# Optimization experiments

Hardware: AMD Instinct MI355X
Metric: run time of the kernel (lower is better)

Reference implementation:

```python
import jax, jax.numpy as jnp
import numpy as np

B, N, K = 16, 2048, 20
EPS = 1e-5
SLOPE = 0.2  # LeakyReLU negative slope


def _lrelu(x):
    return jnp.where(x >= 0, x, SLOPE * x)


def _bn(x, g, b, axes):
    # BatchNorm in training mode (batch statistics), channel-last layout
    m = x.mean(axes, keepdims=True)
    v = x.var(axes, keepdims=True)
    return (x - m) * jax.lax.rsqrt(v + EPS) * g + b


def _graph_features(pts, k):
    # pts: [B, N, C] -> edge features [B, N, k, 2C] = concat(x_j - x_i, x_i)
    xx = jnp.sum(pts * pts, axis=-1)                       # [B, N]
    inner = jnp.einsum('bnc,bmc->bnm', pts, pts)           # [B, N, N]
    neg_d = 2.0 * inner - xx[:, :, None] - xx[:, None, :]  # -||x_i - x_j||^2
    _, idx = jax.lax.top_k(neg_d, k)                       # [B, N, k]
    xj = jax.vmap(lambda p, i: p[i])(pts, idx)             # [B, N, k, C]
    xi = pts[:, :, None, :]                                # [B, N, 1, C]
    return jnp.concatenate([xj - xi, jnp.broadcast_to(xi, xj.shape)], axis=-1)


def _forward(x, conv_w, conv_g, conv_b, w1, b1, g1, bt1, w2, b2, g2, bt2,
             w3, b3, g3, bt3, w4, b4, w5, b5):
    feat = _graph_features(x, K)                           # [B, N, K, 6]
    # 1x1 Conv2d (bias=False) + BN2d + LeakyReLU, then max over neighbors
    h = jnp.einsum('bnkc,oc->bnko', feat, conv_w)          # [B, N, K, 64]
    h = _lrelu(_bn(h, conv_g, conv_b, (0, 1, 2)))
    h = h.max(axis=2)                                      # [B, N, 64]
    # DBR blocks: Linear + BN1d + LeakyReLU over points
    h = _lrelu(_bn(h @ w1 + b1, g1, bt1, (0, 1)))          # [B, N, 64]
    h = _lrelu(_bn(h @ w2 + b2, g2, bt2, (0, 1)))          # [B, N, 128]
    h = _lrelu(_bn(h @ w3 + b3, g3, bt3, (0, 1)))          # [B, N, 128]
    h = h.max(axis=1)                                      # MaxChannel -> [B, 128]
    h = _lrelu(h @ w4 + b4)                                # DbR -> [B, 512]
    return h @ w5 + b5                                     # [B, 2*Z_DIM=256]


def setup_inputs() -> dict:
    key = jax.random.key(0)
    ks = jax.random.split(key, 8)
    rn = lambda k, s, sc: (jax.random.normal(k, s, jnp.float32) * sc)
    return {
        'x': jax.random.normal(ks[0], (B, N, 3), jnp.float32),
        'conv_w': rn(ks[1], (64, 6), 0.3),
        'conv_g': jnp.ones(64, jnp.float32), 'conv_b': jnp.zeros(64, jnp.float32),
        'w1': rn(ks[2], (64, 64), 0.1), 'b1': jnp.zeros(64, jnp.float32),
        'g1': jnp.ones(64, jnp.float32), 'bt1': jnp.zeros(64, jnp.float32),
        'w2': rn(ks[3], (64, 128), 0.1), 'b2': jnp.zeros(128, jnp.float32),
        'g2': jnp.ones(128, jnp.float32), 'bt2': jnp.zeros(128, jnp.float32),
        'w3': rn(ks[4], (128, 128), 0.1), 'b3': jnp.zeros(128, jnp.float32),
        'g3': jnp.ones(128, jnp.float32), 'bt3': jnp.zeros(128, jnp.float32),
        'w4': rn(ks[5], (128, 512), 0.05), 'b4': jnp.zeros(512, jnp.float32),
        'w5': rn(ks[6], (512, 256), 0.05), 'b5': jnp.zeros(256, jnp.float32),
    }


def reference(x, conv_w, conv_g, conv_b, w1, b1, g1, bt1, w2, b2, g2, bt2,
              w3, b3, g3, bt3, w4, b4, w5, b5):
    return _forward(x, conv_w, conv_g, conv_b, w1, b1, g1, bt1, w2, b2, g2, bt2,
                    w3, b3, g3, bt3, w4, b4, w5, b5)
```

## Files before the change

### kernel.cpp

```cpp
#include <hip/hip_runtime.h>
#include <math.h>

#define NB   16
#define NPTS 2048
#define KNBR 20
#define NROWS (NB*NPTS)
#define CONV_M ((double)(NB)*(double)(NPTS)*(double)(KNBR))
#define ROW_M  ((double)NROWS)
#define BN_EPS 1e-5
#define LSLOPE 0.2f

__device__ __forceinline__ float lrelu(float v) { return v >= 0.f ? v : LSLOPE * v; }

__device__ __forceinline__ float4 stage4(float px, float py, float pz)
{
    return make_float4(px + px, py + py, pz + pz,
                       -fmaf(px, px, fmaf(py, py, pz * pz)));
}

__device__ __forceinline__ float dist_eval(float4 q, float4 c)
{
    float t = fmaf(c.x, q.x, fmaf(c.y, q.y, fmaf(c.z, q.z, q.w)));
    return t + c.w;
}

__global__ __launch_bounds__(256) void knn_feat_kernel(const float* __restrict__ x,
        const float* __restrict__ conv_w,
        float* __restrict__ maxh, float* __restrict__ minh, double* __restrict__ S)
{
    __shared__ float4 pts[NPTS];
    __shared__ unsigned short idxl[32][KNBR];
    __shared__ float  featw[4][KNBR][6];
    __shared__ double sred[4][27];
    const int b  = blockIdx.x >> 6;
    const int qg = blockIdx.x & 63;
    const int wv = threadIdx.x >> 6, lane = threadIdx.x & 63;
    const float* xb = x + (size_t)b * NPTS * 3;
    for (int i = threadIdx.x; i < NPTS; i += 256)
        pts[i] = stage4(xb[i*3+0], xb[i*3+1], xb[i*3+2]);
    __syncthreads();

    const unsigned long long below = (1ull << lane) - 1ull;
    for (int qi = 0; qi < 8; ++qi) {
        const int p = wv * 8 + qi;
        const int n = qg * 32 + p;
        const float4 qc = pts[n];
        const float4 q = make_float4(0.5f*qc.x, 0.5f*qc.y, 0.5f*qc.z, qc.w);
        unsigned u[32];
#pragma unroll
        for (int it = 0; it < 32; ++it) {
            float d = dist_eval(q, pts[it*64 + lane]);
            unsigned bits = __float_as_uint(d);
            u[it] = bits ^ (unsigned)(((int)bits >> 31) | (int)0x80000000);
        }
        unsigned lo = 0u, hi = 0xFFFFFFFFu;
        for (int step = 0; step < 32; ++step) {
            const unsigned mid = lo + ((hi - lo) >> 1);
            int cnt = 0;
#pragma unroll
            for (int it = 0; it < 32; ++it)
                cnt += __popcll(__ballot(u[it] >= mid));
            if (cnt == KNBR) {
                unsigned mn = 0xFFFFFFFFu;
#pragma unroll
                for (int it = 0; it < 32; ++it)
                    mn = (u[it] >= mid && u[it] < mn) ? u[it] : mn;
#pragma unroll
                for (int o = 32; o >= 1; o >>= 1) {
                    unsigned other = (unsigned)__shfl_xor((int)mn, o);
                    mn = other < mn ? other : mn;
                }
                lo = mn;
                break;
            }
            if (cnt > KNBR) lo = mid; else hi = mid;
        }
        const unsigned ustar = lo;
        int cnt2 = 0;
#pragma unroll
        for (int it = 0; it < 32; ++it) {
            const bool hit = (u[it] >= ustar);
            unsigned long long mask = __ballot(hit);
            int pos = cnt2 + __popcll(mask & below);
            if (hit && pos < KNBR)
                idxl[p][pos] = (unsigned short)(it*64 + lane);
            cnt2 += __popcll(mask);
        }
    }
    __syncthreads();
    float cw[6];
#pragma unroll
    for (int c = 0; c < 6; ++c) cw[c] = conv_w[lane*6 + c];
    int pa_ = 0, pb_ = 0;
    if (lane >= 6 && lane < 27) {
        int t = lane - 6, a = 0;
        while (t >= 6 - a) { t -= 6 - a; ++a; }
        pa_ = a; pb_ = a + t;
    }
    double acc = 0.0;
    for (int i = 0; i < 8; ++i) {
        const int p = wv * 8 + i;
        const int nn = qg * 32 + p;
        const size_t bp = (size_t)b * NPTS + nn;
        const float4 Ci = pts[nn];
        const float xi0 = 0.5f*Ci.x, xi1 = 0.5f*Ci.y, xi2 = 0.5f*Ci.z;
        float f0=0,f1=0,f2=0,f3=0,f4=0,f5=0;
        if (lane < KNBR) {
            const float4 Cj = pts[idxl[p][lane]];
            f0 = 0.5f*(Cj.x - Ci.x);
            f1 = 0.5f*(Cj.y - Ci.y);
            f2 = 0.5f*(Cj.z - Ci.z);
            f3 = xi0; f4 = xi1; f5 = xi2;
        }
        __syncthreads();
        if (lane < KNBR) {
            featw[wv][lane][0]=f0; featw[wv][lane][1]=f1; featw[wv][lane][2]=f2;
            featw[wv][lane][3]=f3; featw[wv][lane][4]=f4; featw[wv][lane][5]=f5;
        }
        __syncthreads();
        float vmax = -__builtin_inff(), vmin = __builtin_inff();
#pragma unroll
        for (int k = 0; k < KNBR; ++k) {
            float h = featw[wv][k][0] * cw[0];
            h = fmaf(featw[wv][k][1], cw[1], h);
            h = fmaf(featw[wv][k][2], cw[2], h);
            h = fmaf(featw[wv][k][3], cw[3], h);
            h = fmaf(featw[wv][k][4], cw[4], h);
            h = fmaf(featw[wv][k][5], cw[5], h);
            vmax = fmaxf(vmax, h); vmin = fminf(vmin, h);
        }
        maxh[bp*64 + lane] = vmax;
        minh[bp*64 + lane] = vmin;
        if (lane < 6) {
            double s = 0;
#pragma unroll
            for (int k = 0; k < KNBR; ++k) s += (double)featw[wv][k][lane];
            acc += s;
        } else if (lane < 27) {
            double s = 0;
#pragma unroll
            for (int k = 0; k < KNBR; ++k)
                s += (double)featw[wv][k][pa_] * (double)featw[wv][k][pb_];
            acc += s;
        }
    }
    if (lane < 27) sred[wv][lane] = acc;
    __syncthreads();
    if (threadIdx.x < 27) {
        double tot = sred[0][threadIdx.x] + sred[1][threadIdx.x]
                   + sred[2][threadIdx.x] + sred[3][threadIdx.x];
        atomicAdd(&S[threadIdx.x], tot);
    }
}

template<int K, int N, bool SEL, bool POOLOUT, bool STATS0>
__global__ __launch_bounds__(256) void mlp_gemm(const float* __restrict__ A,
        const float* __restrict__ A2,
        const double* __restrict__ st_a, const double* __restrict__ st_b,
        const float* __restrict__ st_g, const float* __restrict__ st_bt,
        const float* __restrict__ cwm,
        const float* __restrict__ W, const float* __restrict__ bias,
        float* __restrict__ Y, double* __restrict__ sum, double* __restrict__ sq,
        float* __restrict__ pmax_g, float* __restrict__ pmin_g)
{
    constexpr int CPT = N / 16;
    __shared__ float As[64 * 64];
    __shared__ float Ws[64 * N];
    __shared__ __align__(16) float s_scale[K], s_shift[K];
    const int tid = threadIdx.x;
    if (tid < K) {
        const int o = tid;
        if (STATS0) {
            double w[6];
#pragma unroll
            for (int c = 0; c < 6; ++c) w[c] = (double)cwm[o*6 + c];
            double mean = 0.0;
#pragma unroll
            for (int c = 0; c < 6; ++c) mean += w[c] * st_a[c];
            mean /= CONV_M;
            double ey2 = 0.0;
            int t = 6;
#pragma unroll
            for (int a = 0; a < 6; ++a)
#pragma unroll
                for (int b2 = a; b2 < 6; ++b2) {
                    double coef = (a == b2) ? 1.0 : 2.0;
                    ey2 += coef * w[a] * w[b2] * st_a[t];
                    ++t;
                }
            ey2 /= CONV_M;
            double var = ey2 - mean * mean;
            double sc = (double)st_g[o] / sqrt(var + BN_EPS);
            s_scale[o] = (float)sc;
            s_shift[o] = (float)((double)st_bt[o] - mean * sc);
        } else {
            double m = st_a[o] / ROW_M;
            double v = st_b[o] / ROW_M - m * m;
            double sc = (double)st_g[o] / sqrt(v + BN_EPS);
            s_scale[o] = (float)sc;
            s_shift[o] = (float)((double)st_bt[o] - m * sc);
        }
    }
    const int row0 = blockIdx.x * 64;
    const int ct = tid & 15, rt = tid >> 4;
    float acc[4][CPT];
#pragma unroll
    for (int rr = 0; rr < 4; ++rr)
#pragma unroll
        for (int cc = 0; cc < CPT; ++cc) acc[rr][cc] = bias[ct*CPT + cc];
    __syncthreads();

    for (int kk = 0; kk < K/64; ++kk) {
        if (kk) __syncthreads();
#pragma unroll
        for (int i = 0; i < 4; ++i) {
            const int f   = i * 256 + tid;
            const int k4  = f & 15;
            const int row = f >> 4;
            const int kg  = kk*64 + k4*4;
            float4 m = *(const float4*)(A + (size_t)(row0+row)*K + kg);
            const float4 s4 = *(const float4*)(&s_scale[kg]);
            const float4 h4 = *(const float4*)(&s_shift[kg]);
            if (SEL) {
                float4 m2 = *(const float4*)(A2 + (size_t)(row0+row)*K + kg);
                m.x = s4.x >= 0.f ? m.x : m2.x;
                m.y = s4.y >= 0.f ? m.y : m2.y;
                m.z = s4.z >= 0.f ? m.z : m2.z;
                m.w = s4.w >= 0.f ? m.w : m2.w;
            }
            const int rsw = row ^ ((k4 & 7) << 2);
            As[(k4*4+0)*64 + rsw] = lrelu(fmaf(s4.x, m.x, h4.x));
            As[(k4*4+1)*64 + rsw] = lrelu(fmaf(s4.y, m.y, h4.y));
            As[(k4*4+2)*64 + rsw] = lrelu(fmaf(s4.z, m.z, h4.z));
            As[(k4*4+3)*64 + rsw] = lrelu(fmaf(s4.w, m.w, h4.w));
        }
#pragma unroll
        for (int i = 0; i < N/16; ++i) {
            const int f    = i * 256 + tid;
            const int col4 = f & (N/4 - 1);
            const int krow = f / (N/4);
            *(float4*)(&Ws[krow*N + col4*4]) =
                *(const float4*)(W + (size_t)(kk*64 + krow)*N + col4*4);
        }
        __syncthreads();
#pragma unroll 4
        for (int k = 0; k < 64; ++k) {
            const int sw = ((k >> 2) & 7) << 2;
            const float4 a0 = *(const float4*)(&As[k*64 + ((rt*4) ^ sw)]);
            float a_[4] = {a0.x, a0.y, a0.z, a0.w};
            float w_[CPT];
#pragma unroll
            for (int v = 0; v < CPT/4; ++v) {
                const float4 wv4 = *(const float4*)(&Ws[k*N + ct*CPT + v*4]);
                w_[v*4+0] = wv4.x; w_[v*4+1] = wv4.y; w_[v*4+2] = wv4.z; w_[v*4+3] = wv4.w;
            }
#pragma unroll
            for (int rr = 0; rr < 4; ++rr)
#pragma unroll
                for (int cc = 0; cc < CPT; ++cc)
                    acc[rr][cc] = fmaf(a_[rr], w_[cc], acc[rr][cc]);
        }
    }
    if (!POOLOUT) {
#pragma unroll
        for (int rr = 0; rr < 4; ++rr) {
            float* yo = Y + (size_t)(row0 + rt*4 + rr)*N + ct*CPT;
#pragma unroll
            for (int v = 0; v < CPT/4; ++v)
                *(float4*)(yo + v*4) = make_float4(acc[rr][v*4+0], acc[rr][v*4+1],
                                                   acc[rr][v*4+2], acc[rr][v*4+3]);
        }
    }
    __syncthreads();
    float* cr  = As;
    float* pmx = As + 512;
    float* pmn = Ws;
    if (tid < 2*N) cr[tid] = 0.f;
    if (POOLOUT) {
#pragma unroll
        for (int cc = 0; cc < CPT; ++cc) {
            float vmax = fmaxf(fmaxf(acc[0][cc], acc[1][cc]), fmaxf(acc[2][cc], acc[3][cc]));
            float vmin = fminf(fminf(acc[0][cc], acc[1][cc]), fminf(acc[2][cc], acc[3][cc]));
            pmx[rt*N + ct*CPT + cc] = vmax;
            pmn[rt*N + ct*CPT + cc] = vmin;
        }
    }
    __syncthreads();
#pragma unroll
    for (int cc = 0; cc < CPT; ++cc) {
        float s = acc[0][cc] + acc[1][cc] + acc[2][cc] + acc[3][cc];
        float q = fmaf(acc[0][cc], acc[0][cc], 0.f);
        q = fmaf(acc[1][cc], acc[1][cc], q);
        q = fmaf(acc[2][cc], acc[2][cc], q);
        q = fmaf(acc[3][cc], acc[3][cc], q);
        atomicAdd(&cr[ct*CPT + cc], s);
        atomicAdd(&cr[N + ct*CPT + cc], q);
    }
    float rm = 0.f, rn = 0.f;
    if (POOLOUT && tid < N) {
        rm = pmx[tid]; rn = pmn[tid];
#pragma unroll
        for (int r = 1; r < 16; ++r) {
            rm = fmaxf(rm, pmx[r*N + tid]);
            rn = fminf(rn, pmn[r*N + tid]);
        }
    }
    __syncthreads();
    if (tid < N) {
        atomicAdd(&sum[tid], (double)cr[tid]);
        atomicAdd(&sq[tid],  (double)cr[N + tid]);
        if (POOLOUT) {
            pmax_g[(size_t)blockIdx.x * N + tid] = rm;
            pmin_g[(size_t)blockIdx.x * N + tid] = rn;
        }
    }
}

__global__ __launch_bounds__(256) void headpool_kernel(const float* __restrict__ pmax_g,
        const float* __restrict__ pmin_g,
        const double* __restrict__ sum3, const double* __restrict__ sq3,
        const float* __restrict__ g3, const float* __restrict__ bt3,
        const float* __restrict__ w4, const float* __restrict__ b4,
        const float* __restrict__ w5, const float* __restrict__ b5,
        float* __restrict__ out)
{
    __shared__ float xr[128];
    __shared__ float hh[512];
    const int b = blockIdx.x, t = threadIdx.x;
    if (t < 128) {
        double m_ = sum3[t] / ROW_M;
        double v_ = sq3[t] / ROW_M - m_ * m_;
        double scd = (double)g3[t] / sqrt(v_ + BN_EPS);
        const float sc = (float)scd;
        const float sh = (float)((double)bt3[t] - m_ * scd);
        const float* pm = pmax_g + (size_t)b * 32 * 128 + t;
        const float* pn = pmin_g + (size_t)b * 32 * 128 + t;
        float m = pm[0], n_ = pn[0];
#pragma unroll
        for (int r = 1; r < 32; ++r) {
            m  = fmaxf(m,  pm[r*128]);
            n_ = fminf(n_, pn[r*128]);
        }
        xr[t] = lrelu(sc >= 0.f ? fmaf(sc, m, sh) : fmaf(sc, n_, sh));
    }
    __syncthreads();
    float h0 = b4[t], h1 = b4[t + 256];
    for (int c = 0; c < 128; ++c) {
        float xc = xr[c];
        h0 = fmaf(xc, w4[c*512 + t],       h0);
        h1 = fmaf(xc, w4[c*512 + t + 256], h1);
    }
    hh[t]       = lrelu(h0);
    hh[t + 256] = lrelu(h1);
    __syncthreads();
    float acc = b5[t];
    for (int c = 0; c < 512; ++c)
        acc = fmaf(hh[c], w5[c*256 + t], acc);
    out[b*256 + t] = acc;
}

extern "C" void kernel_launch(void* const* d_in, const int* in_sizes, int n_in,
                              void* d_out, int out_size, void* d_ws, size_t ws_size,
                              hipStream_t stream)
{
    const float* x      = (const float*)d_in[0];
    const float* conv_w = (const float*)d_in[1];
    const float* conv_g = (const float*)d_in[2];
    const float* conv_b = (const float*)d_in[3];
    const float* w1  = (const float*)d_in[4];
    const float* b1  = (const float*)d_in[5];
    const float* g1  = (const float*)d_in[6];
    const float* bt1 = (const float*)d_in[7];
    const float* w2  = (const float*)d_in[8];
    const float* b2  = (const float*)d_in[9];
    const float* g2  = (const float*)d_in[10];
    const float* bt2 = (const float*)d_in[11];
    const float* w3  = (const float*)d_in[12];
    const float* b3  = (const float*)d_in[13];
    const float* g3  = (const float*)d_in[14];
    const float* bt3 = (const float*)d_in[15];
    const float* w4  = (const float*)d_in[16];
    const float* b4  = (const float*)d_in[17];
    const float* w5  = (const float*)d_in[18];
    const float* b5  = (const float*)d_in[19];

    char* p = (char*)d_ws;
    auto take = [&](size_t bytes) -> char* {
        char* r = p; p += (bytes + 255) & ~(size_t)255; return r;
    };
    double* S    = (double*)take(27 * 8);
    double* sum1 = (double*)take(64 * 8);
    double* sq1  = (double*)take(64 * 8);
    double* sum2 = (double*)take(128 * 8);
    double* sq2  = (double*)take(128 * 8);
    double* sum3 = (double*)take(128 * 8);
    double* sq3  = (double*)take(128 * 8);
    size_t zero_bytes = (size_t)(p - (char*)d_ws);
    float* pmaxg  = (float*)take((size_t)512 * 128 * 4);
    float* pming  = (float*)take((size_t)512 * 128 * 4);
    float* mm     = (float*)take((size_t)NROWS * 128 * 4);
    float* maxh   = mm;
    float* minh   = mm + (size_t)NROWS * 64;
    float* y1     = (float*)take((size_t)NROWS * 64 * 4);
    float* y2     = (float*)take((size_t)NROWS * 128 * 4);

    hipMemsetAsync(d_ws, 0, zero_bytes, stream);
    knn_feat_kernel<<<dim3(NB * 64), dim3(256), 0, stream>>>(x, conv_w, maxh, minh, S);

    mlp_gemm<64,64,true,false,true>    <<<dim3(512), dim3(256), 0, stream>>>(
        maxh, minh, S, nullptr, conv_g, conv_b, conv_w, w1, b1, y1, sum1, sq1, nullptr, nullptr);
    mlp_gemm<64,128,false,false,false> <<<dim3(512), dim3(256), 0, stream>>>(
        y1, y1, sum1, sq1, g1, bt1, nullptr, w2, b2, y2, sum2, sq2, nullptr, nullptr);
    mlp_gemm<128,128,false,true,false> <<<dim3(512), dim3(256), 0, stream>>>(
        y2, y2, sum2, sq2, g2, bt2, nullptr, w3, b3, nullptr, sum3, sq3, pmaxg, pming);

    headpool_kernel<<<dim3(NB), dim3(256), 0, stream>>>(
        pmaxg, pming, sum3, sq3, g3, bt3, w4, b4, w5, b5, (float*)d_out);
}
```

Measured before the change: 391.5 us.

## Replace radix bisection top-k with per-thread sorted insertion and threshold merge

The kNN threshold search drops the 32-step bitwise bisection over ballots. In its place, each query is split across 8 threads. Each thread keeps a register-resident sorted list of its 20 best distances, using min/med3/max pair insertion with a shared threshold and buffered candidates. The lists are merged across the 8 threads by butterfly shuffles, and the resulting 20th-best value is passed through shared memory to a single ballot pass that writes indices. This removes many ballot/popcount reductions, at the cost of higher register pressure, divergence, and a second distance evaluation pass.

```diff
diff --git a/kernel.cpp b/kernel.cpp
--- a/kernel.cpp
+++ b/kernel.cpp
@@ -24,6 +24,19 @@
     return t + c.w;
 }
 
+__device__ __forceinline__ void pair_insert_sorted(float (&bestv)[KNBR], float t0, float t1)
+{
+#pragma unroll
+    for (int j = 0; j < KNBR; ++j) {
+        float bj = bestv[j];
+        float nb  = fmaxf(bj, t0);
+        float nt0 = __builtin_amdgcn_fmed3f(bj, t0, t1);
+        float nt1 = fminf(bj, t1);
+        bestv[j] = nb;
+        t0 = nt0; t1 = nt1;
+    }
+}
+
 __global__ __launch_bounds__(256) void knn_feat_kernel(const float* __restrict__ x,
         const float* __restrict__ conv_w,
         float* __restrict__ maxh, float* __restrict__ minh, double* __restrict__ S)
@@ -32,62 +45,99 @@
     __shared__ unsigned short idxl[32][KNBR];
     __shared__ float  featw[4][KNBR][6];
     __shared__ double sred[4][27];
+    __shared__ float  tbuf[32];
     const int b  = blockIdx.x >> 6;
     const int qg = blockIdx.x & 63;
-    const int wv = threadIdx.x >> 6, lane = threadIdx.x & 63;
     const float* xb = x + (size_t)b * NPTS * 3;
     for (int i = threadIdx.x; i < NPTS; i += 256)
         pts[i] = stage4(xb[i*3+0], xb[i*3+1], xb[i*3+2]);
     __syncthreads();
 
+    {
+        const int qi = threadIdx.x >> 3;
+        const int c  = threadIdx.x & 7;
+        const int n  = qg * 32 + qi;
+        const float4 qc = pts[n];
+        const float4 q = make_float4(0.5f*qc.x, 0.5f*qc.y, 0.5f*qc.z, qc.w);
+        const int cbase = c * 256;
+        const int rot   = (37 * c) & 255;
+        float bestv[KNBR];
+#pragma unroll
+        for (int j = 0; j < KNBR; ++j) bestv[j] = -__builtin_inff();
+        for (int m = 0; m < 64; m += 2) {
+            const int j0 = (m + rot) & 255;
+            const int j1 = (j0 + 1) & 255;
+            float d0 = dist_eval(q, pts[cbase + j0]);
+            float d1 = dist_eval(q, pts[cbase + j1]);
+            pair_insert_sorted(bestv, fmaxf(d0, d1), fminf(d0, d1));
+        }
+        float L = bestv[KNBR-1];
+        L = fmaxf(L, __shfl_xor(L, 1));
+        L = fmaxf(L, __shfl_xor(L, 2));
+        L = fmaxf(L, __shfl_xor(L, 4));
+#pragma unroll
+        for (int j = 0; j < KNBR; ++j) bestv[j] = fmaxf(bestv[j], L);
+        float thresh = bestv[KNBR-1];
+        float r0 = -__builtin_inff(), r1 = r0, r2 = r0, r3 = r0;
+        int rc = 0;
+        for (int m = 64; m < 256; m += 2) {
+            const int j0 = (m + rot) & 255;
+            const int j1 = (j0 + 1) & 255;
+            float d0 = dist_eval(q, pts[cbase + j0]);
+            float d1 = dist_eval(q, pts[cbase + j1]);
+            bool h0 = d0 > thresh;
+            r3 = h0 ? r2 : r3; r2 = h0 ? r1 : r2; r1 = h0 ? r0 : r1; r0 = h0 ? d0 : r0;
+            rc += h0 ? 1 : 0;
+            bool h1 = d1 > thresh;
+            r3 = h1 ? r2 : r3; r2 = h1 ? r1 : r2; r1 = h1 ? r0 : r1; r0 = h1 ? d1 : r0;
+            rc += h1 ? 1 : 0;
+            if (__any(rc >= 3)) {
+                pair_insert_sorted(bestv, fmaxf(r0, r1), fminf(r0, r1));
+                pair_insert_sorted(bestv, fmaxf(r2, r3), fminf(r2, r3));
+                r0 = r1 = r2 = r3 = -__builtin_inff();
+                rc = 0;
+                thresh = bestv[KNBR-1];
+            }
+        }
+        pair_insert_sorted(bestv, fmaxf(r0, r1), fminf(r0, r1));
+        pair_insert_sorted(bestv, fmaxf(r2, r3), fminf(r2, r3));
+#pragma unroll
+        for (int lev = 1; lev <= 4; lev <<= 1) {
+            float orig[KNBR];
+#pragma unroll
+            for (int j = 0; j < KNBR; ++j) orig[j] = bestv[j];
+            for (int i = 0; i < KNBR; i += 2) {
+                float nb0 = __shfl_xor(orig[i],   lev);
+                float nb1 = __shfl_xor(orig[i+1], lev);
+                if (!__any(nb0 > bestv[KNBR-1])) break;
+                pair_insert_sorted(bestv, nb0, nb1);
+            }
+        }
+        if (c == 0) tbuf[qi] = bestv[KNBR-1];
+    }
+    __syncthreads();
+
+    const int wv = threadIdx.x >> 6, lane = threadIdx.x & 63;
     const unsigned long long below = (1ull << lane) - 1ull;
-    for (int qi = 0; qi < 8; ++qi) {
-        const int p = wv * 8 + qi;
+    for (int qi2 = 0; qi2 < 8; ++qi2) {
+        const int p = wv * 8 + qi2;
         const int n = qg * 32 + p;
         const float4 qc = pts[n];
         const float4 q = make_float4(0.5f*qc.x, 0.5f*qc.y, 0.5f*qc.z, qc.w);
-        unsigned u[32];
-#pragma unroll
+        const float th = tbuf[p];
+        int cnt = 0;
         for (int it = 0; it < 32; ++it) {
             float d = dist_eval(q, pts[it*64 + lane]);
-            unsigned bits = __float_as_uint(d);
-            u[it] = bits ^ (unsigned)(((int)bits >> 31) | (int)0x80000000);
-        }
-        unsigned lo = 0u, hi = 0xFFFFFFFFu;
-        for (int step = 0; step < 32; ++step) {
-            const unsigned mid = lo + ((hi - lo) >> 1);
-            int cnt = 0;
-#pragma unroll
-            for (int it = 0; it < 32; ++it)
-                cnt += __popcll(__ballot(u[it] >= mid));
-            if (cnt == KNBR) {
-                unsigned mn = 0xFFFFFFFFu;
-#pragma unroll
-                for (int it = 0; it < 32; ++it)
-                    mn = (u[it] >= mid && u[it] < mn) ? u[it] : mn;
-#pragma unroll
-                for (int o = 32; o >= 1; o >>= 1) {
-                    unsigned other = (unsigned)__shfl_xor((int)mn, o);
-                    mn = other < mn ? other : mn;
-                }
-                lo = mn;
-                break;
-            }
-            if (cnt > KNBR) lo = mid; else hi = mid;
-        }
-        const unsigned ustar = lo;
-        int cnt2 = 0;
-#pragma unroll
-        for (int it = 0; it < 32; ++it) {
-            const bool hit = (u[it] >= ustar);
+            const bool hit = (d >= th);
             unsigned long long mask = __ballot(hit);
-            int pos = cnt2 + __popcll(mask & below);
+            int pos = cnt + __popcll(mask & below);
             if (hit && pos < KNBR)
                 idxl[p][pos] = (unsigned short)(it*64 + lane);
-            cnt2 += __popcll(mask);
-        }
-    }
-    __syncthreads();
+            cnt += __popcll(mask);
+        }
+    }
+    __syncthreads();
+
     float cw[6];
 #pragma unroll
     for (int c = 0; c < 6; ++c) cw[c] = conv_w[lane*6 + c];
```

New measurement: 342.8 us. -12.4%, faster.

## Replace radix binary-search top-k with wave-wide bitonic sort/merge threshold selection

Applied to the files above, without the earlier changes.

The k-NN threshold is no longer found by a 32-step binary search over per-lane keys with ballot counts. Each wave now keeps a running top-64 state across lanes, using bitonic sort and merge built from DPP-free shuffles. A chunk is merged only when some lane beats the current minimum, and the 20th largest value becomes the threshold. Distances are recomputed in a second pass to gather the indices. This cuts register pressure and the ballot-heavy search, at the cost of shuffle-heavy sorting and duplicated distance evaluation.

```diff
diff --git a/kernel.cpp b/kernel.cpp
--- a/kernel.cpp
+++ b/kernel.cpp
@@ -24,6 +24,61 @@
     return t + c.w;
 }
 
+constexpr unsigned long long km_asc(int k, int j) {
+    unsigned long long m = 0;
+    for (int l = 0; l < 64; ++l) {
+        bool up = ((l & k) == 0);
+        bool km = up ? ((l & j) != 0) : ((l & j) == 0);
+        if (km) m |= 1ull << l;
+    }
+    return m;
+}
+constexpr unsigned long long km_mrg(int j) {
+    unsigned long long m = 0;
+    for (int l = 0; l < 64; ++l)
+        if ((l & j) == 0) m |= 1ull << l;
+    return m;
+}
+
+template<unsigned long long KM>
+__device__ __forceinline__ float cex_stage(float v, int j)
+{
+    float p = __shfl_xor(v, j);
+    float mn = fminf(v, p), mx = fmaxf(v, p);
+    float r;
+    asm("v_cndmask_b32 %0, %1, %2, %3" : "=v"(r) : "v"(mn), "v"(mx), "s"(KM));
+    return r;
+}
+
+__device__ __forceinline__ float sort64_asc(float v)
+{
+    v = cex_stage<km_asc(2,1)>(v,1);
+    v = cex_stage<km_asc(4,2)>(v,2);   v = cex_stage<km_asc(4,1)>(v,1);
+    v = cex_stage<km_asc(8,4)>(v,4);   v = cex_stage<km_asc(8,2)>(v,2);
+    v = cex_stage<km_asc(8,1)>(v,1);
+    v = cex_stage<km_asc(16,8)>(v,8);  v = cex_stage<km_asc(16,4)>(v,4);
+    v = cex_stage<km_asc(16,2)>(v,2);  v = cex_stage<km_asc(16,1)>(v,1);
+    v = cex_stage<km_asc(32,16)>(v,16);v = cex_stage<km_asc(32,8)>(v,8);
+    v = cex_stage<km_asc(32,4)>(v,4);  v = cex_stage<km_asc(32,2)>(v,2);
+    v = cex_stage<km_asc(32,1)>(v,1);
+    v = cex_stage<km_asc(64,32)>(v,32);v = cex_stage<km_asc(64,16)>(v,16);
+    v = cex_stage<km_asc(64,8)>(v,8);  v = cex_stage<km_asc(64,4)>(v,4);
+    v = cex_stage<km_asc(64,2)>(v,2);  v = cex_stage<km_asc(64,1)>(v,1);
+    return v;
+}
+__device__ __forceinline__ float merge64_desc(float v)
+{
+    v = cex_stage<km_mrg(32)>(v,32); v = cex_stage<km_mrg(16)>(v,16);
+    v = cex_stage<km_mrg(8)>(v,8);   v = cex_stage<km_mrg(4)>(v,4);
+    v = cex_stage<km_mrg(2)>(v,2);   v = cex_stage<km_mrg(1)>(v,1);
+    return v;
+}
+
+__device__ __forceinline__ float lane_read(float v, int l)
+{
+    return __uint_as_float(__builtin_amdgcn_readlane(__float_as_uint(v), l));
+}
+
 __global__ __launch_bounds__(256) void knn_feat_kernel(const float* __restrict__ x,
         const float* __restrict__ conv_w,
         float* __restrict__ maxh, float* __restrict__ minh, double* __restrict__ S)
@@ -32,6 +87,7 @@
     __shared__ unsigned short idxl[32][KNBR];
     __shared__ float  featw[4][KNBR][6];
     __shared__ double sred[4][27];
+    __shared__ float  tbuf[32];
     const int b  = blockIdx.x >> 6;
     const int qg = blockIdx.x & 63;
     const int wv = threadIdx.x >> 6, lane = threadIdx.x & 63;
@@ -40,54 +96,45 @@
         pts[i] = stage4(xb[i*3+0], xb[i*3+1], xb[i*3+2]);
     __syncthreads();
 
-    const unsigned long long below = (1ull << lane) - 1ull;
     for (int qi = 0; qi < 8; ++qi) {
         const int p = wv * 8 + qi;
         const int n = qg * 32 + p;
         const float4 qc = pts[n];
         const float4 q = make_float4(0.5f*qc.x, 0.5f*qc.y, 0.5f*qc.z, qc.w);
-        unsigned u[32];
-#pragma unroll
+        float state = -__builtin_inff();
         for (int it = 0; it < 32; ++it) {
             float d = dist_eval(q, pts[it*64 + lane]);
-            unsigned bits = __float_as_uint(d);
-            u[it] = bits ^ (unsigned)(((int)bits >> 31) | (int)0x80000000);
-        }
-        unsigned lo = 0u, hi = 0xFFFFFFFFu;
-        for (int step = 0; step < 32; ++step) {
-            const unsigned mid = lo + ((hi - lo) >> 1);
-            int cnt = 0;
-#pragma unroll
-            for (int it = 0; it < 32; ++it)
-                cnt += __popcll(__ballot(u[it] >= mid));
-            if (cnt == KNBR) {
-                unsigned mn = 0xFFFFFFFFu;
-#pragma unroll
-                for (int it = 0; it < 32; ++it)
-                    mn = (u[it] >= mid && u[it] < mn) ? u[it] : mn;
-#pragma unroll
-                for (int o = 32; o >= 1; o >>= 1) {
-                    unsigned other = (unsigned)__shfl_xor((int)mn, o);
-                    mn = other < mn ? other : mn;
-                }
-                lo = mn;
-                break;
+            float smin = lane_read(state, 63);
+            if (__any(d > smin)) {
+                float nv = sort64_asc(d);
+                state = fmaxf(state, nv);
+                state = merge64_desc(state);
             }
-            if (cnt > KNBR) lo = mid; else hi = mid;
-        }
-        const unsigned ustar = lo;
-        int cnt2 = 0;
-#pragma unroll
+        }
+        if (lane == 0) tbuf[p] = lane_read(state, 19);
+    }
+    __syncthreads();
+
+    const unsigned long long below = (1ull << lane) - 1ull;
+    for (int qi2 = 0; qi2 < 8; ++qi2) {
+        const int p = wv * 8 + qi2;
+        const int n = qg * 32 + p;
+        const float4 qc = pts[n];
+        const float4 q = make_float4(0.5f*qc.x, 0.5f*qc.y, 0.5f*qc.z, qc.w);
+        const float th = tbuf[p];
+        int cnt = 0;
         for (int it = 0; it < 32; ++it) {
-            const bool hit = (u[it] >= ustar);
+            float d = dist_eval(q, pts[it*64 + lane]);
+            const bool hit = (d >= th);
             unsigned long long mask = __ballot(hit);
-            int pos = cnt2 + __popcll(mask & below);
+            int pos = cnt + __popcll(mask & below);
             if (hit && pos < KNBR)
                 idxl[p][pos] = (unsigned short)(it*64 + lane);
-            cnt2 += __popcll(mask);
-        }
-    }
-    __syncthreads();
+            cnt += __popcll(mask);
+        }
+    }
+    __syncthreads();
+
     float cw[6];
 #pragma unroll
     for (int c = 0; c < 6; ++c) cw[c] = conv_w[lane*6 + c];
```

Result: slower. 798.8 us (+104.1%).
